# Performance work log

Hardware: AMD Instinct MI355X
Metric: run time of the kernel (lower is better)

Reference implementation:

```python
import jax, jax.numpy as jnp
import numpy as np
from jax import lax

ALPHA = 2.0        # elastic_alpha per axis
SMOOTH_NUM = 4
WIN = 5            # box smoothing window
FS = 11            # elastic field size per dim
SIZE_O = (128, 128, 128)


def _rodrigues(rot):
    # rot: (N,3) angle-axis -> (N,3,3) rotation matrix, with Taylor fallback near 0
    eps = 1e-6
    theta2 = jnp.sum(rot * rot, axis=1, keepdims=True)            # (N,1)
    theta = jnp.sqrt(jnp.maximum(theta2, eps))                    # safe sqrt
    w = rot / (theta + eps)
    wx, wy, wz = w[:, 0:1], w[:, 1:2], w[:, 2:3]
    c = jnp.cos(theta)
    s = jnp.sin(theta)
    k = 1.0 - c
    Rn = jnp.concatenate([
        c + wx * wx * k, wx * wy * k - wz * s, wy * s + wx * wz * k,
        wz * s + wx * wy * k, c + wy * wy * k, -wx * s + wy * wz * k,
        -wy * s + wx * wz * k, wx * s + wy * wz * k, c + wz * wz * k,
    ], axis=1).reshape(-1, 3, 3)
    rx, ry, rz = rot[:, 0:1], rot[:, 1:2], rot[:, 2:3]
    one = jnp.ones_like(rx)
    Rt = jnp.concatenate([one, -rz, ry, rz, one, -rx, -ry, rx, one],
                         axis=1).reshape(-1, 3, 3)
    mask = (theta2 > eps)[:, :, None]                             # (N,1,1)
    return jnp.where(mask, Rn, Rt)


def _box_smooth(d):
    # replicate-pad + mean box filter (torch __smooth_3d__)
    p = WIN // 2
    dp = jnp.pad(d, ((0, 0), (0, 0), (p, p), (p, p), (p, p)), mode='edge')
    k = jnp.ones((1, 1, WIN, WIN, WIN), d.dtype) / float(WIN ** 3)
    return lax.conv_general_dilated(dp, k, (1, 1, 1), 'VALID',
                                    dimension_numbers=('NCDHW', 'OIDHW', 'NCDHW'))


def _resize1d(x, axis, out_size):
    # linear interpolation along one axis, align_corners=False (torch interpolate)
    in_size = x.shape[axis]
    src = (jnp.arange(out_size, dtype=x.dtype) + 0.5) * (in_size / out_size) - 0.5
    src = jnp.clip(src, 0.0, in_size - 1.0)
    i0 = jnp.floor(src).astype(jnp.int32)
    i1 = jnp.minimum(i0 + 1, in_size - 1)
    w = (src - i0.astype(x.dtype))
    shape = [1] * x.ndim
    shape[axis] = out_size
    w = w.reshape(shape)
    x0 = jnp.take(x, i0, axis=axis)
    x1 = jnp.take(x, i1, axis=axis)
    return x0 * (1.0 - w) + x1 * w


def _resize3d(d, size):
    d = _resize1d(d, 2, size[0])
    d = _resize1d(d, 3, size[1])
    d = _resize1d(d, 4, size[2])
    return d


def _grid_sample3d(vol, grid):
    # vol: (N,C,D,H,W), grid: (N,D,H,W,3) normalized (x,y,z); trilinear, zeros pad,
    # align_corners=False (torch grid_sample defaults)
    N, C, D, H, W = vol.shape
    x = ((grid[..., 0] + 1.0) * W - 1.0) * 0.5
    y = ((grid[..., 1] + 1.0) * H - 1.0) * 0.5
    z = ((grid[..., 2] + 1.0) * D - 1.0) * 0.5
    x0f, y0f, z0f = jnp.floor(x), jnp.floor(y), jnp.floor(z)
    wx, wy, wz = x - x0f, y - y0f, z - z0f
    x0 = x0f.astype(jnp.int32)
    y0 = y0f.astype(jnp.int32)
    z0 = z0f.astype(jnp.int32)
    b = jnp.arange(N)[:, None, None, None]

    def gather(zi, yi, xi):
        valid = (zi >= 0) & (zi < D) & (yi >= 0) & (yi < H) & (xi >= 0) & (xi < W)
        v = vol[b, :, jnp.clip(zi, 0, D - 1), jnp.clip(yi, 0, H - 1),
                jnp.clip(xi, 0, W - 1)]                           # (N,Do,Ho,Wo,C)
        return v * valid[..., None].astype(vol.dtype)

    out = (gather(z0, y0, x0) * ((1 - wz) * (1 - wy) * (1 - wx))[..., None]
           + gather(z0, y0, x0 + 1) * ((1 - wz) * (1 - wy) * wx)[..., None]
           + gather(z0, y0 + 1, x0) * ((1 - wz) * wy * (1 - wx))[..., None]
           + gather(z0, y0 + 1, x0 + 1) * ((1 - wz) * wy * wx)[..., None]
           + gather(z0 + 1, y0, x0) * (wz * (1 - wy) * (1 - wx))[..., None]
           + gather(z0 + 1, y0, x0 + 1) * (wz * (1 - wy) * wx)[..., None]
           + gather(z0 + 1, y0 + 1, x0) * (wz * wy * (1 - wx))[..., None]
           + gather(z0 + 1, y0 + 1, x0 + 1) * (wz * wy * wx)[..., None])
    return jnp.transpose(out, (0, 4, 1, 2, 3))


def _field(raw, size):
    # raw uniform field -> scaled, smoothed, cropped, resized displacement (D,H,W)
    d = (raw - 0.5) * 2.0 * ALPHA
    for _ in range(SMOOTH_NUM):
        d = _box_smooth(d)
    p = WIN // 2
    d = d[:, :, p:p + FS, p:p + FS, p:p + FS]
    return _resize3d(d, size)[0, 0]


def _forward(vol, rot, scale, shift, dz, dy, dx):
    N, C, D, H, W = vol.shape
    R = _rodrigues(rot)                                  # (N,3,3)
    A = R * scale[:, None, :]                            # scale multiplies columns
    theta = jnp.concatenate([A, shift[:, :, None]], axis=2)  # (N,3,4)
    # base affine grid, align_corners=False: coord_i = (2i+1)/S - 1
    xs = (2.0 * jnp.arange(W, dtype=vol.dtype) + 1.0) / W - 1.0
    ys = (2.0 * jnp.arange(H, dtype=vol.dtype) + 1.0) / H - 1.0
    zs = (2.0 * jnp.arange(D, dtype=vol.dtype) + 1.0) / D - 1.0
    zz, yy, xx = jnp.meshgrid(zs, ys, xs, indexing='ij')
    pts = jnp.stack([xx, yy, zz, jnp.ones_like(xx)], axis=-1)    # (D,H,W,4)
    grid = jnp.einsum('nij,dhwj->ndhwi', theta, pts)             # (N,D,H,W,3)
    disp = jnp.stack([_field(dz, (D, H, W)), _field(dy, (D, H, W)),
                      _field(dx, (D, H, W))], axis=-1)           # (D,H,W,3)
    grid = grid + disp[None]
    out = _grid_sample3d(vol, grid)
    # central crop to SIZE_O
    zs0 = D // 2 - SIZE_O[0] // 2
    ys0 = H // 2 - SIZE_O[1] // 2
    xs0 = W // 2 - SIZE_O[2] // 2
    return out[:, :, zs0:zs0 + SIZE_O[0], ys0:ys0 + SIZE_O[1], xs0:xs0 + SIZE_O[2]]


def setup_inputs() -> dict:
    key = jax.random.key(0)
    k = jax.random.split(key, 7)
    vol = jax.random.normal(k[0], (4, 1, 160, 160, 160), dtype=jnp.float32)
    rot = (jax.random.uniform(k[1], (4, 3), dtype=jnp.float32) - 0.5) * 0.35   # ~±10 deg in rad
    scale = 0.9 + 0.2 * jax.random.uniform(k[2], (4, 3), dtype=jnp.float32)
    shift = (jax.random.uniform(k[3], (4, 3), dtype=jnp.float32) - 0.5) * 0.1
    dz = jax.random.uniform(k[4], (1, 1, 15, 15, 15), dtype=jnp.float32)
    dy = jax.random.uniform(k[5], (1, 1, 15, 15, 15), dtype=jnp.float32)
    dx = jax.random.uniform(k[6], (1, 1, 15, 15, 15), dtype=jnp.float32)
    return {"vol": vol, "rot": rot, "scale": scale, "shift": shift,
            "dz": dz, "dy": dy, "dx": dx}


def reference(vol, rot, scale, shift, dz, dy, dx):
    return _forward(vol, rot, scale, shift, dz, dy, dx)
```

## Files before the change

kernel.cpp:

```cpp
#include <hip/hip_runtime.h>
#include <hip/hip_bf16.h>

#define VD 160
#define OD 128
#define CROP0 16
#define FSZ 11
#define RAWSZ 15
#define NBATCH 4
#define ODQ 4

#define ESTR 17
#define EOH  (8*ESTR)
#define ECH  (8*8*ESTR)

__global__ __launch_bounds__(256) void prep_kernel(
        const float* __restrict__ rot, const float* __restrict__ scale,
        const float* __restrict__ shift,
        const float* __restrict__ dz, const float* __restrict__ dy,
        const float* __restrict__ dx,
        float* __restrict__ theta, float* __restrict__ fields) {
    const int tid = threadIdx.x;
    const int chan = blockIdx.x;

    if (chan == 3) {
        int n = tid;
        if (n >= NBATCH) return;
        float rx = rot[n*3+0], ry = rot[n*3+1], rz = rot[n*3+2];
        float t2 = rx*rx + ry*ry + rz*rz;
        const float eps = 1e-6f;
        float th = sqrtf(fmaxf(t2, eps));
        float inv = 1.0f / (th + eps);
        float wx = rx*inv, wy = ry*inv, wz = rz*inv;
        float c = cosf(th), s = sinf(th), k = 1.0f - c;
        float R[9];
        if (t2 > eps) {
            R[0] = c + wx*wx*k;      R[1] = wx*wy*k - wz*s;  R[2] = wy*s + wx*wz*k;
            R[3] = wz*s + wx*wy*k;   R[4] = c + wy*wy*k;     R[5] = -wx*s + wy*wz*k;
            R[6] = -wy*s + wx*wz*k;  R[7] = wx*s + wy*wz*k;  R[8] = c + wz*wz*k;
        } else {
            R[0] = 1.0f; R[1] = -rz;  R[2] = ry;
            R[3] = rz;   R[4] = 1.0f; R[5] = -rx;
            R[6] = -ry;  R[7] = rx;   R[8] = 1.0f;
        }
        for (int i = 0; i < 3; ++i) {
            for (int j = 0; j < 3; ++j)
                theta[n*12 + i*4 + j] = R[i*3 + j] * scale[n*3 + j];
            theta[n*12 + i*4 + 3] = shift[n*3 + i];
        }
        return;
    }

    __shared__ float bufA[RAWSZ*RAWSZ*RAWSZ];
    __shared__ float bufB[RAWSZ*RAWSZ*RAWSZ];
    const float* raw = (chan == 0) ? dz : (chan == 1) ? dy : dx;
    const int NTOT = RAWSZ*RAWSZ*RAWSZ;

    for (int i = tid; i < NTOT; i += 256)
        bufA[i] = (raw[i] - 0.5f) * 4.0f;
    __syncthreads();

    float* src = bufA;
    float* dst = bufB;
    for (int it = 0; it < 4; ++it) {
        for (int ax = 0; ax < 3; ++ax) {
            const int stride = (ax == 0) ? RAWSZ*RAWSZ : (ax == 1) ? RAWSZ : 1;
            for (int i = tid; i < NTOT; i += 256) {
                int z = i / (RAWSZ*RAWSZ);
                int r = i % (RAWSZ*RAWSZ);
                int y = r / RAWSZ;
                int x = r % RAWSZ;
                int c = (ax == 0) ? z : (ax == 1) ? y : x;
                float s = 0.0f;
                #pragma unroll
                for (int t = -2; t <= 2; ++t) {
                    int cc = min(max(c + t, 0), RAWSZ - 1);
                    s += src[i + (cc - c) * stride];
                }
                dst[i] = s * 0.2f;
            }
            __syncthreads();
            float* tmp = src; src = dst; dst = tmp;
        }
    }
    for (int i = tid; i < FSZ*FSZ*FSZ; i += 256) {
        int z = i / (FSZ*FSZ);
        int r = i % (FSZ*FSZ);
        int y = r / FSZ;
        int x = r % FSZ;
        fields[chan*FSZ*FSZ*FSZ + i] =
            src[(z+2)*RAWSZ*RAWSZ + (y+2)*RAWSZ + (x+2)];
    }
}

__device__ __forceinline__ void resize_coord(int m, int& i0, int& i1, float& w) {
    float s = fmaf((float)m + 0.5f, (float)FSZ / (float)VD, -0.5f);
    s = fminf(fmaxf(s, 0.0f), (float)(FSZ - 1));
    float f = floorf(s);
    i0 = (int)f;
    i1 = min(i0 + 1, FSZ - 1);
    w = s - f;
}

__global__ __launch_bounds__(512) void sample_kernel(
        const float* __restrict__ vol, const float* __restrict__ theta,
        const float* __restrict__ fields, float* __restrict__ out) {
    __shared__ float e[3*ECH];

    const int tid  = threadIdx.x;
    const int lane = tid & 63;
    const int wl   = lane & 15;
    const int hl   = lane >> 4;
    const int wv   = tid >> 6;
    const int wx   = wv & 1;
    const int wh   = (wv >> 1) & 1;
    const int wd   = wv >> 2;

    const int ow_l = (wx << 4) | wl;
    const int oh_l = (wh << 2) | hl;
    const int ow   = (blockIdx.x << 5) | ow_l;
    const int oh   = (blockIdx.y << 3) | oh_l;
    const int odb  = (blockIdx.z & 15) << 3;
    const int n    = blockIdx.z >> 4;

    #pragma unroll
    for (int i = 0; i < 6; ++i) {
        const int t = tid + (i << 9);
        const int xi  = t & 15;
        const int row = t >> 4;
        if (xi < FSZ) {
            const int c   = row >> 6;
            const int r   = row & 63;
            const int eoh = r >> 3;
            const int eod = r & 7;
            int d_ = odb + eod + CROP0;
            int h_ = (blockIdx.y << 3) + eoh + CROP0;
            int zi0, zi1, yi0, yi1;
            float zw, yw;
            resize_coord(d_, zi0, zi1, zw);
            resize_coord(h_, yi0, yi1, yw);
            const float* f = fields + c * (FSZ*FSZ*FSZ);
            float v = f[zi0*121 + yi0*11 + xi] * ((1.0f-zw)*(1.0f-yw))
                    + f[zi0*121 + yi1*11 + xi] * ((1.0f-zw)*yw)
                    + f[zi1*121 + yi0*11 + xi] * (zw*(1.0f-yw))
                    + f[zi1*121 + yi1*11 + xi] * (zw*yw);
            e[row*ESTR + xi] = v * 80.0f;
        }
    }
    __syncthreads();

    const int w_ = ow + CROP0;
    const int h_ = oh + CROP0;

    const float x = fmaf(2.0f * (float)w_ + 1.0f, 1.0f / (float)VD, -1.0f);
    const float y = fmaf(2.0f * (float)h_ + 1.0f, 1.0f / (float)VD, -1.0f);

    float s = fmaf((float)w_ + 0.5f, (float)FSZ / (float)VD, -0.5f);
    s = fminf(fmaxf(s, 0.0f), (float)(FSZ - 1));
    const float sf = floorf(s);
    const int   xi0 = (int)sf;
    const float xw  = s - sf;

    const float* th = theta + n*12;
    const float cx = fmaf(th[0]*x + th[1]*y + th[3], 80.0f, 79.5f);
    const float cy = fmaf(th[4]*x + th[5]*y + th[7], 80.0f, 79.5f);
    const float cz = fmaf(th[8]*x + th[9]*y + th[11], 80.0f, 79.5f);
    const float tz0 = th[2] * 80.0f, tz1 = th[6] * 80.0f, tz2 = th[10] * 80.0f;

    const float* v = vol + (size_t)n * (VD*VD*VD);

    const float* ebase = &e[oh_l*EOH + (wd << 2)*ESTR + xi0];

    #pragma unroll
    for (int k = 0; k < ODQ; ++k) {
        const int od = odb + ((wd << 2) | k);
        const int d_ = od + CROP0;
        const float z = fmaf(2.0f * (float)d_ + 1.0f, 1.0f / (float)VD, -1.0f);

        const float ex0 = ebase[        k*ESTR    ], ex1 = ebase[        k*ESTR + 1];
        const float ey0 = ebase[ECH   + k*ESTR    ], ey1 = ebase[ECH   + k*ESTR + 1];
        const float ez0 = ebase[2*ECH + k*ESTR    ], ez1 = ebase[2*ECH + k*ESTR + 1];
        const float d80x = fmaf(ex1 - ex0, xw, ex0);
        const float d80y = fmaf(ey1 - ey0, xw, ey0);
        const float d80z = fmaf(ez1 - ez0, xw, ez0);

        const float xs = fmaf(tz0, z, cx) + d80x;
        const float ys = fmaf(tz1, z, cy) + d80y;
        const float zs = fmaf(tz2, z, cz) + d80z;

        const float x0f = floorf(xs), y0f = floorf(ys), z0f = floorf(zs);
        const float fx = xs - x0f, fy = ys - y0f, fz = zs - z0f;
        const int ix0 = (int)x0f, iy0 = (int)y0f, iz0 = (int)z0f;
        const int ix1 = ix0 + 1,  iy1 = iy0 + 1,  iz1 = iz0 + 1;

        const float WX0 = ((unsigned)ix0 < (unsigned)VD) ? (1.0f - fx) : 0.0f;
        const float WX1 = ((unsigned)ix1 < (unsigned)VD) ? fx          : 0.0f;
        const float WY0 = ((unsigned)iy0 < (unsigned)VD) ? (1.0f - fy) : 0.0f;
        const float WY1 = ((unsigned)iy1 < (unsigned)VD) ? fy          : 0.0f;
        const float WZ0 = ((unsigned)iz0 < (unsigned)VD) ? (1.0f - fz) : 0.0f;
        const float WZ1 = ((unsigned)iz1 < (unsigned)VD) ? fz          : 0.0f;

        const int xc0 = min(max(ix0, 0), VD-1), xc1 = min(max(ix1, 0), VD-1);
        const int yc0 = min(max(iy0, 0), VD-1), yc1 = min(max(iy1, 0), VD-1);
        const int zc0 = min(max(iz0, 0), VD-1), zc1 = min(max(iz1, 0), VD-1);

        const int base = min(xc0, VD-2);
        const bool hi0 = (xc0 != base);
        const bool hi1 = (xc1 != base);
        const float wA = (hi0 ? 0.0f : WX0) + (hi1 ? 0.0f : WX1);
        const float wB = (hi0 ? WX0 : 0.0f) + (hi1 ? WX1 : 0.0f);

        const int b00 = (zc0*VD + yc0)*VD + base;
        const int b01 = (zc0*VD + yc1)*VD + base;
        const int b10 = (zc1*VD + yc0)*VD + base;
        const int b11 = (zc1*VD + yc1)*VD + base;

        float2 p00, p01, p10, p11;
        __builtin_memcpy(&p00, v + b00, sizeof(float2));
        __builtin_memcpy(&p01, v + b01, sizeof(float2));
        __builtin_memcpy(&p10, v + b10, sizeof(float2));
        __builtin_memcpy(&p11, v + b11, sizeof(float2));

        const float r00 = p00.x*wA + p00.y*wB;
        const float r01 = p01.x*wA + p01.y*wB;
        const float r10 = p10.x*wA + p10.y*wB;
        const float r11 = p11.x*wA + p11.y*wB;
        const float r = (r00*WY0 + r01*WY1)*WZ0 + (r10*WY0 + r11*WY1)*WZ1;

        out[(((size_t)n*OD + od)*OD + oh)*OD + ow] = r;
    }
}

extern "C" void kernel_launch(void* const* d_in, const int* in_sizes, int n_in,
                              void* d_out, int out_size, void* d_ws, size_t ws_size,
                              hipStream_t stream) {
    const float* vol   = (const float*)d_in[0];
    const float* rot   = (const float*)d_in[1];
    const float* scale = (const float*)d_in[2];
    const float* shift = (const float*)d_in[3];
    const float* dz    = (const float*)d_in[4];
    const float* dy    = (const float*)d_in[5];
    const float* dx    = (const float*)d_in[6];
    float* out = (float*)d_out;

    float* ws     = (float*)d_ws;
    float* theta  = ws;
    float* fields = ws + 48;

    prep_kernel<<<4, 256, 0, stream>>>(rot, scale, shift, dz, dy, dx,
                                       theta, fields);
    dim3 grid(OD/32, OD/8, (OD/8)*NBATCH);
    sample_kernel<<<grid, 512, 0, stream>>>(vol, theta, fields, out);
}
```

Measured before the change: 160.2 us.

## Add wave-uniform interior fast path for trilinear sampling and widen prep kernel

Widens the prep kernel to 1024 threads with precomputed per-thread coordinates, so the serial smoothing passes need fewer iterations and no repeated div/mod. The elastic-field staging now computes resize weights once per thread and reuses them across channels. In the sampler, when every lane of a wave is strictly inside the volume, a simplified lerp path skips clamping and weight masking. Output addressing and z are computed incrementally. The costs are branch divergence and more code, and the fast path only applies when a whole wave is in bounds.

```diff
diff --git a/kernel.cpp b/kernel.cpp
--- a/kernel.cpp
+++ b/kernel.cpp
@@ -13,7 +13,7 @@
 #define EOH  (8*ESTR)
 #define ECH  (8*8*ESTR)
 
-__global__ __launch_bounds__(256) void prep_kernel(
+__global__ __launch_bounds__(1024) void prep_kernel(
         const float* __restrict__ rot, const float* __restrict__ scale,
         const float* __restrict__ shift,
         const float* __restrict__ dz, const float* __restrict__ dy,
@@ -55,38 +55,53 @@
     const float* raw = (chan == 0) ? dz : (chan == 1) ? dy : dx;
     const int NTOT = RAWSZ*RAWSZ*RAWSZ;
 
-    for (int i = tid; i < NTOT; i += 256)
+    for (int i = tid; i < NTOT; i += 1024)
         bufA[i] = (raw[i] - 0.5f) * 4.0f;
+
+    int cz[4], cy[4], cxx[4];
+    bool val[4];
+    #pragma unroll
+    for (int j = 0; j < 4; ++j) {
+        const int i = tid + j*1024;
+        val[j] = (i < NTOT);
+        const int ii = val[j] ? i : 0;
+        cz[j]  = ii / (RAWSZ*RAWSZ);
+        const int r = ii % (RAWSZ*RAWSZ);
+        cy[j]  = r / RAWSZ;
+        cxx[j] = r % RAWSZ;
+    }
     __syncthreads();
 
     float* src = bufA;
     float* dst = bufB;
     for (int it = 0; it < 4; ++it) {
+        #pragma unroll
         for (int ax = 0; ax < 3; ++ax) {
             const int stride = (ax == 0) ? RAWSZ*RAWSZ : (ax == 1) ? RAWSZ : 1;
-            for (int i = tid; i < NTOT; i += 256) {
-                int z = i / (RAWSZ*RAWSZ);
-                int r = i % (RAWSZ*RAWSZ);
-                int y = r / RAWSZ;
-                int x = r % RAWSZ;
-                int c = (ax == 0) ? z : (ax == 1) ? y : x;
-                float s = 0.0f;
-                #pragma unroll
-                for (int t = -2; t <= 2; ++t) {
-                    int cc = min(max(c + t, 0), RAWSZ - 1);
-                    s += src[i + (cc - c) * stride];
+            #pragma unroll
+            for (int j = 0; j < 4; ++j) {
+                if (val[j]) {
+                    const int i = tid + j*1024;
+                    const int c = (ax == 0) ? cz[j] : (ax == 1) ? cy[j] : cxx[j];
+                    const int ib = i - c*stride;
+                    float s = 0.0f;
+                    #pragma unroll
+                    for (int t = -2; t <= 2; ++t) {
+                        const int cc = min(max(c + t, 0), RAWSZ - 1);
+                        s += src[ib + cc*stride];
+                    }
+                    dst[i] = s * 0.2f;
                 }
-                dst[i] = s * 0.2f;
             }
             __syncthreads();
             float* tmp = src; src = dst; dst = tmp;
         }
     }
-    for (int i = tid; i < FSZ*FSZ*FSZ; i += 256) {
-        int z = i / (FSZ*FSZ);
-        int r = i % (FSZ*FSZ);
-        int y = r / FSZ;
-        int x = r % FSZ;
+    for (int i = tid; i < FSZ*FSZ*FSZ; i += 1024) {
+        const int z = i / (FSZ*FSZ);
+        const int r = i % (FSZ*FSZ);
+        const int y = r / FSZ;
+        const int x = r % FSZ;
         fields[chan*FSZ*FSZ*FSZ + i] =
             src[(z+2)*RAWSZ*RAWSZ + (y+2)*RAWSZ + (x+2)];
     }
@@ -122,28 +137,38 @@
     const int odb  = (blockIdx.z & 15) << 3;
     const int n    = blockIdx.z >> 4;
 
-    #pragma unroll
-    for (int i = 0; i < 6; ++i) {
-        const int t = tid + (i << 9);
-        const int xi  = t & 15;
-        const int row = t >> 4;
+    {
+        const int xi   = tid & 15;
+        const int row0 = tid >> 4;
         if (xi < FSZ) {
-            const int c   = row >> 6;
-            const int r   = row & 63;
-            const int eoh = r >> 3;
-            const int eod = r & 7;
-            int d_ = odb + eod + CROP0;
-            int h_ = (blockIdx.y << 3) + eoh + CROP0;
-            int zi0, zi1, yi0, yi1;
-            float zw, yw;
-            resize_coord(d_, zi0, zi1, zw);
-            resize_coord(h_, yi0, yi1, yw);
-            const float* f = fields + c * (FSZ*FSZ*FSZ);
-            float v = f[zi0*121 + yi0*11 + xi] * ((1.0f-zw)*(1.0f-yw))
-                    + f[zi0*121 + yi1*11 + xi] * ((1.0f-zw)*yw)
-                    + f[zi1*121 + yi0*11 + xi] * (zw*(1.0f-yw))
-                    + f[zi1*121 + yi1*11 + xi] * (zw*yw);
-            e[row*ESTR + xi] = v * 80.0f;
+            const int eod  = row0 & 7;
+            const int eoh0 = row0 >> 3;
+            int zi0, zi1, yA0, yA1, yB0, yB1;
+            float zw, ywA, ywB;
+            resize_coord(odb + eod + CROP0, zi0, zi1, zw);
+            const int hbase = (blockIdx.y << 3) + CROP0;
+            resize_coord(hbase + eoh0,     yA0, yA1, ywA);
+            resize_coord(hbase + eoh0 + 4, yB0, yB1, ywB);
+            const float wz0 = 1.0f - zw;
+            const float wA00 = wz0*(1.0f-ywA), wA01 = wz0*ywA;
+            const float wA10 = zw*(1.0f-ywA),  wA11 = zw*ywA;
+            const float wB00 = wz0*(1.0f-ywB), wB01 = wz0*ywB;
+            const float wB10 = zw*(1.0f-ywB),  wB11 = zw*ywB;
+            const int oA00 = zi0*121 + yA0*11 + xi, oA01 = zi0*121 + yA1*11 + xi;
+            const int oA10 = zi1*121 + yA0*11 + xi, oA11 = zi1*121 + yA1*11 + xi;
+            const int oB00 = zi0*121 + yB0*11 + xi, oB01 = zi0*121 + yB1*11 + xi;
+            const int oB10 = zi1*121 + yB0*11 + xi, oB11 = zi1*121 + yB1*11 + xi;
+            float* ew = &e[row0*ESTR + xi];
+            #pragma unroll
+            for (int i = 0; i < 6; ++i) {
+                const float* f = fields + (i >> 1) * (FSZ*FSZ*FSZ);
+                float v;
+                if (i & 1)
+                    v = f[oB00]*wB00 + f[oB01]*wB01 + f[oB10]*wB10 + f[oB11]*wB11;
+                else
+                    v = f[oA00]*wA00 + f[oA01]*wA01 + f[oA10]*wA10 + f[oA11]*wA11;
+                ew[i * (32*ESTR)] = v * 80.0f;
+            }
         }
     }
     __syncthreads();
@@ -170,11 +195,13 @@
 
     const float* ebase = &e[oh_l*EOH + (wd << 2)*ESTR + xi0];
 
+    const int dbase = odb + (wd << 2) + CROP0;
+    const float zb = fmaf(2.0f * (float)dbase + 1.0f, 1.0f / (float)VD, -1.0f);
+    float* op = out + ((((size_t)n*OD + (odb + (wd << 2)))*OD + oh)*OD + ow);
+
     #pragma unroll
     for (int k = 0; k < ODQ; ++k) {
-        const int od = odb + ((wd << 2) | k);
-        const int d_ = od + CROP0;
-        const float z = fmaf(2.0f * (float)d_ + 1.0f, 1.0f / (float)VD, -1.0f);
+        const float z = zb + (float)k * (2.0f / (float)VD);
 
         const float ex0 = ebase[        k*ESTR    ], ex1 = ebase[        k*ESTR + 1];
         const float ey0 = ebase[ECH   + k*ESTR    ], ey1 = ebase[ECH   + k*ESTR + 1];
@@ -190,43 +217,62 @@
         const float x0f = floorf(xs), y0f = floorf(ys), z0f = floorf(zs);
         const float fx = xs - x0f, fy = ys - y0f, fz = zs - z0f;
         const int ix0 = (int)x0f, iy0 = (int)y0f, iz0 = (int)z0f;
-        const int ix1 = ix0 + 1,  iy1 = iy0 + 1,  iz1 = iz0 + 1;
-
-        const float WX0 = ((unsigned)ix0 < (unsigned)VD) ? (1.0f - fx) : 0.0f;
-        const float WX1 = ((unsigned)ix1 < (unsigned)VD) ? fx          : 0.0f;
-        const float WY0 = ((unsigned)iy0 < (unsigned)VD) ? (1.0f - fy) : 0.0f;
-        const float WY1 = ((unsigned)iy1 < (unsigned)VD) ? fy          : 0.0f;
-        const float WZ0 = ((unsigned)iz0 < (unsigned)VD) ? (1.0f - fz) : 0.0f;
-        const float WZ1 = ((unsigned)iz1 < (unsigned)VD) ? fz          : 0.0f;
-
-        const int xc0 = min(max(ix0, 0), VD-1), xc1 = min(max(ix1, 0), VD-1);
-        const int yc0 = min(max(iy0, 0), VD-1), yc1 = min(max(iy1, 0), VD-1);
-        const int zc0 = min(max(iz0, 0), VD-1), zc1 = min(max(iz1, 0), VD-1);
-
-        const int base = min(xc0, VD-2);
-        const bool hi0 = (xc0 != base);
-        const bool hi1 = (xc1 != base);
-        const float wA = (hi0 ? 0.0f : WX0) + (hi1 ? 0.0f : WX1);
-        const float wB = (hi0 ? WX0 : 0.0f) + (hi1 ? WX1 : 0.0f);
-
-        const int b00 = (zc0*VD + yc0)*VD + base;
-        const int b01 = (zc0*VD + yc1)*VD + base;
-        const int b10 = (zc1*VD + yc0)*VD + base;
-        const int b11 = (zc1*VD + yc1)*VD + base;
-
-        float2 p00, p01, p10, p11;
-        __builtin_memcpy(&p00, v + b00, sizeof(float2));
-        __builtin_memcpy(&p01, v + b01, sizeof(float2));
-        __builtin_memcpy(&p10, v + b10, sizeof(float2));
-        __builtin_memcpy(&p11, v + b11, sizeof(float2));
-
-        const float r00 = p00.x*wA + p00.y*wB;
-        const float r01 = p01.x*wA + p01.y*wB;
-        const float r10 = p10.x*wA + p10.y*wB;
-        const float r11 = p11.x*wA + p11.y*wB;
-        const float r = (r00*WY0 + r01*WY1)*WZ0 + (r10*WY0 + r11*WY1)*WZ1;
-
-        out[(((size_t)n*OD + od)*OD + oh)*OD + ow] = r;
+
+        float r;
+        const int inb = ((unsigned)ix0 < (unsigned)(VD-1)) &
+                        ((unsigned)iy0 < (unsigned)(VD-1)) &
+                        ((unsigned)iz0 < (unsigned)(VD-1));
+        if (__all(inb)) {
+            const int b00 = (iz0*VD + iy0)*VD + ix0;
+            float2 p00, p01, p10, p11;
+            __builtin_memcpy(&p00, v + b00,             sizeof(float2));
+            __builtin_memcpy(&p01, v + b00 + VD,        sizeof(float2));
+            __builtin_memcpy(&p10, v + b00 + VD*VD,     sizeof(float2));
+            __builtin_memcpy(&p11, v + b00 + VD*VD+VD,  sizeof(float2));
+            const float r00 = fmaf(fx, p00.y - p00.x, p00.x);
+            const float r01 = fmaf(fx, p01.y - p01.x, p01.x);
+            const float r10 = fmaf(fx, p10.y - p10.x, p10.x);
+            const float r11 = fmaf(fx, p11.y - p11.x, p11.x);
+            const float r0 = fmaf(fy, r01 - r00, r00);
+            const float r1 = fmaf(fy, r11 - r10, r10);
+            r = fmaf(fz, r1 - r0, r0);
+        } else {
+            const int ix1 = ix0 + 1,  iy1 = iy0 + 1,  iz1 = iz0 + 1;
+
+            const float WX0 = ((unsigned)ix0 < (unsigned)VD) ? (1.0f - fx) : 0.0f;
+            const float WX1 = ((unsigned)ix1 < (unsigned)VD) ? fx          : 0.0f;
+            const float WY0 = ((unsigned)iy0 < (unsigned)VD) ? (1.0f - fy) : 0.0f;
+            const float WY1 = ((unsigned)iy1 < (unsigned)VD) ? fy          : 0.0f;
+            const float WZ0 = ((unsigned)iz0 < (unsigned)VD) ? (1.0f - fz) : 0.0f;
+            const float WZ1 = ((unsigned)iz1 < (unsigned)VD) ? fz          : 0.0f;
+
+            const int xc0 = min(max(ix0, 0), VD-1), xc1 = min(max(ix1, 0), VD-1);
+            const int yc0 = min(max(iy0, 0), VD-1), yc1 = min(max(iy1, 0), VD-1);
+            const int zc0 = min(max(iz0, 0), VD-1), zc1 = min(max(iz1, 0), VD-1);
+
+            const int base = min(xc0, VD-2);
+            const bool hi0 = (xc0 != base);
+            const bool hi1 = (xc1 != base);
+            const float wA = (hi0 ? 0.0f : WX0) + (hi1 ? 0.0f : WX1);
+            const float wB = (hi0 ? WX0 : 0.0f) + (hi1 ? WX1 : 0.0f);
+
+            const int sA = zc0*(VD*VD), sB = zc1*(VD*VD);
+            const int tA = yc0*VD + base, tB = yc1*VD + base;
+
+            float2 p00, p01, p10, p11;
+            __builtin_memcpy(&p00, v + sA + tA, sizeof(float2));
+            __builtin_memcpy(&p01, v + sA + tB, sizeof(float2));
+            __builtin_memcpy(&p10, v + sB + tA, sizeof(float2));
+            __builtin_memcpy(&p11, v + sB + tB, sizeof(float2));
+
+            const float r00 = p00.x*wA + p00.y*wB;
+            const float r01 = p01.x*wA + p01.y*wB;
+            const float r10 = p10.x*wA + p10.y*wB;
+            const float r11 = p11.x*wA + p11.y*wB;
+            r = (r00*WY0 + r01*WY1)*WZ0 + (r10*WY0 + r11*WY1)*WZ1;
+        }
+
+        op[(size_t)k*OD*OD] = r;
     }
 }
 
@@ -246,8 +292,8 @@
     float* theta  = ws;
     float* fields = ws + 48;
 
-    prep_kernel<<<4, 256, 0, stream>>>(rot, scale, shift, dz, dy, dx,
-                                       theta, fields);
+    prep_kernel<<<4, 1024, 0, stream>>>(rot, scale, shift, dz, dy, dx,
+                                        theta, fields);
     dim3 grid(OD/32, OD/8, (OD/8)*NBATCH);
     sample_kernel<<<grid, 512, 0, stream>>>(vol, theta, fields, out);
 }
```

New measurement: 145.0 us. 9.5% less time.
